# Optimization experiments

Hardware: AMD Instinct MI355X
Metric: run time of the kernel (lower is better)

## Reference

```python
import jax, jax.numpy as jnp
import numpy as np

NSTEP = 5

# Clauses (vals = one-hot satisfying truth value per literal):
#   clause 0: ~S(x) | C(x)          vals: L0=[1,0], L1=[0,1]
#   clause 1: ~F(x,y) | ~S(x) | S(y) vals: L0=[1,0], L1=[1,0], L2=[0,1]
# Message to target literal i (torch influence()):
#   msg = w[r] * einsum over shared vars of prod_j ( q[pn_j] . (1 - vals_j) ) outer t_vals

def setup_inputs() -> dict:
    B, N = 2, 2048
    key = jax.random.key(0)
    k1, k2, k3 = jax.random.split(key, 3)
    return {
        "logits_S": jax.random.normal(k1, (B, N, 2), jnp.float32),
        "logits_C": jax.random.normal(k2, (B, N, 2), jnp.float32),
        "logits_F": jax.random.normal(k3, (B, N, N, 2), jnp.float32),
        "weights": jnp.ones((2,), jnp.float32),
    }


def _messages(qS, qC, qF, weights):
    dt = qS.dtype
    e_true = jnp.array([0.0, 1.0], dtype=dt)   # one-hot: positive literal satisfied
    e_false = jnp.array([1.0, 0.0], dtype=dt)  # one-hot: negated literal satisfied
    w0, w1 = weights[0], weights[1]
    # clause 0: ~S(x) | C(x)
    msg_C = (w0 * qS[..., 1])[..., None] * e_true            # [B,N,2]
    msg_S = (w0 * qC[..., 0])[..., None] * e_false           # [B,N,2]
    # clause 1: ~F(x,y) | ~S(x) | S(y)
    # target F(x,y): (q_S[b,x,true]) * (q_S[b,y,false]) on the 'false' slot of F
    msg_F = (w1 * qS[:, :, None, 1] * qS[:, None, :, 0])[..., None] * e_false  # [B,N,N,2]
    # target ~S(x): sum_y q_F[b,x,y,true] * q_S[b,y,false]
    msg_S = msg_S + (w1 * jnp.einsum('bxy,by->bx', qF[..., 1], qS[..., 0]))[..., None] * e_false
    # target S(y): sum_x q_F[b,x,y,true] * q_S[b,x,true]
    msg_S = msg_S + (w1 * jnp.einsum('bxy,bx->by', qF[..., 1], qS[..., 1]))[..., None] * e_true
    return msg_S, msg_C, msg_F


def reference(logits_S, logits_C, logits_F, weights):
    cur_S, cur_C, cur_F = logits_S, logits_C, logits_F
    for _ in range(NSTEP):
        qS = jax.nn.softmax(cur_S, axis=-1)
        qC = jax.nn.softmax(cur_C, axis=-1)
        qF = jax.nn.softmax(cur_F, axis=-1)
        msg_S, msg_C, msg_F = _messages(qS, qC, qF, weights)
        cur_S = logits_S + msg_S
        cur_C = logits_C + msg_C
        cur_F = logits_F + msg_F
    return (cur_S, cur_C, cur_F)
```

## Files before the change

### kernel.cpp

```cpp
#include <hip/hip_runtime.h>

#define BB 2
#define NN 2048
#define ROWS (BB*NN)
#define RPB 16
#define CSPLIT 4

__device__ __forceinline__ float fsig(float x) {
    float e = __expf(-x);
    return __builtin_amdgcn_rcpf(1.0f + e);
}

__global__ void ksmall(const float* __restrict__ S, const float* __restrict__ C,
                       const float* __restrict__ w,
                       float* __restrict__ r, float* __restrict__ c,
                       const float* __restrict__ aS_prev, float* __restrict__ aS_cur,
                       float* __restrict__ qC0, int first)
{
    int idx = blockIdx.x * blockDim.x + threadIdx.x;
    if (idx >= ROWS) return;
    float w0 = w[0], w1 = w[1];
    float S0 = S[2*idx], S1 = S[2*idx+1];
    float C0 = C[2*idx], C1 = C[2*idx+1];
    float aS, qc;
    if (first) {
        aS = fsig(S1 - S0);
        qc = fsig(C0 - C1);
    } else {
        float ap  = aS_prev[idx];
        float qcp = qC0[idx];
        float s0 = S0 + w0*qcp + w1*r[idx];
        float s1 = S1 + w1*c[idx];
        aS = fsig(s1 - s0);
        qc = fsig(C0 - C1 - w0*ap);
    }
    aS_cur[idx] = aS;
    qC0[idx]    = qc;
    r[idx]      = 0.0f;
    c[idx]      = 0.0f;
}

template<int MODE>
__global__ __launch_bounds__(256) void kbig(
    const float4* __restrict__ F,
    const float* __restrict__ aS_cur, const float* __restrict__ aS_prev,
    const float* __restrict__ w,
    float* __restrict__ r, float* __restrict__ c,
    float4* __restrict__ outF)
{
    const int tid  = threadIdx.x;
    const int j    = blockIdx.x * 256 + tid;
    const int row0 = blockIdx.y * RPB;
    const int b    = row0 >> 11;
    const int lane = tid & 63;
    const float w1 = w[1];

    const float wq0 = 1.0f - aS_cur[b*NN + 2*j];
    const float wq1 = 1.0f - aS_cur[b*NN + 2*j + 1];
    float bp0 = 0.0f, bp1 = 0.0f;
    if (MODE != 0) {
        bp0 = 1.0f - aS_prev[b*NN + 2*j];
        bp1 = 1.0f - aS_prev[b*NN + 2*j + 1];
    }

    float c0 = 0.0f, c1 = 0.0f;

#pragma unroll 2
    for (int i = 0; i < RPB; i++) {
        const int row = row0 + i;
        const int x   = row & (NN - 1);
        const float a_c = aS_cur[b*NN + x];
        float m1 = 0.0f;
        if (MODE != 0) m1 = w1 * aS_prev[b*NN + x];

        const float4 f = F[(size_t)row * (NN/2) + j];
        const float d0 = f.y - f.x;
        const float d1 = f.w - f.z;
        float s0, s1;
        if (MODE == 0) { s0 = fsig(d0); s1 = fsig(d1); }
        else           { s0 = fsig(d0 - m1*bp0); s1 = fsig(d1 - m1*bp1); }

        c0 += s0 * a_c;
        c1 += s1 * a_c;

        if (MODE == 2) {
            const float mw = w1 * a_c;
            float4 o;
            o.x = f.x + mw*wq0;
            o.y = f.y;
            o.z = f.z + mw*wq1;
            o.w = f.w;
            outF[(size_t)row * (NN/2) + j] = o;
        }

        float ra = s0*wq0 + s1*wq1;
#pragma unroll
        for (int off = 32; off > 0; off >>= 1) ra += __shfl_down(ra, off);
        if (lane == 0) atomicAdd(&r[row], ra);
    }

    atomicAdd(&c[b*NN + 2*j],     c0);
    atomicAdd(&c[b*NN + 2*j + 1], c1);
}

__global__ void kfin(const float* __restrict__ S, const float* __restrict__ C,
                     const float* __restrict__ w,
                     const float* __restrict__ r, const float* __restrict__ c,
                     const float* __restrict__ aS4, const float* __restrict__ qC0,
                     float* __restrict__ outS, float* __restrict__ outC)
{
    int idx = blockIdx.x * blockDim.x + threadIdx.x;
    if (idx >= ROWS) return;
    float w0 = w[0], w1 = w[1];
    outS[2*idx]   = S[2*idx]   + w0*qC0[idx] + w1*r[idx];
    outS[2*idx+1] = S[2*idx+1] + w1*c[idx];
    outC[2*idx]   = C[2*idx];
    outC[2*idx+1] = C[2*idx+1] + w0*aS4[idx];
}

extern "C" void kernel_launch(void* const* d_in, const int* in_sizes, int n_in,
                              void* d_out, int out_size, void* d_ws, size_t ws_size,
                              hipStream_t stream)
{
    const float* S = (const float*)d_in[0];
    const float* C = (const float*)d_in[1];
    const float* F = (const float*)d_in[2];
    const float* w = (const float*)d_in[3];
    float* out = (float*)d_out;
    float* ws  = (float*)d_ws;

    float* aSA = ws;
    float* aSB = ws + ROWS;
    float* qC0 = ws + 2*ROWS;
    float* r   = ws + 3*ROWS;
    float* c   = ws + 4*ROWS;

    const float4* F4 = (const float4*)F;
    float* outS = out;
    float* outC = out + 2*ROWS;
    float4* outF = (float4*)(out + 4*ROWS);

    dim3 gs(ROWS/256), bs(256);
    dim3 gb(CSPLIT, ROWS/RPB), bbk(256);

    ksmall<<<gs, bs, 0, stream>>>(S, C, w, r, c, aSB, aSA, qC0, 1);
    kbig<0><<<gb, bbk, 0, stream>>>(F4, aSA, aSB, w, r, c, nullptr);
    ksmall<<<gs, bs, 0, stream>>>(S, C, w, r, c, aSA, aSB, qC0, 0);
    kbig<1><<<gb, bbk, 0, stream>>>(F4, aSB, aSA, w, r, c, nullptr);
    ksmall<<<gs, bs, 0, stream>>>(S, C, w, r, c, aSB, aSA, qC0, 0);
    kbig<1><<<gb, bbk, 0, stream>>>(F4, aSA, aSB, w, r, c, nullptr);
    ksmall<<<gs, bs, 0, stream>>>(S, C, w, r, c, aSA, aSB, qC0, 0);
    kbig<1><<<gb, bbk, 0, stream>>>(F4, aSB, aSA, w, r, c, nullptr);
    ksmall<<<gs, bs, 0, stream>>>(S, C, w, r, c, aSB, aSA, qC0, 0);
    kbig<2><<<gb, bbk, 0, stream>>>(F4, aSA, aSB, w, r, c, outF);
    kfin<<<gs, bs, 0, stream>>>(S, C, w, r, c, aSA, qC0, outS, outC);
}
```

Before: 222.3 us.

## Fuse all iterations into one cooperative kernel caching F differences in LDS

Replaces the eleven launches with a single cooperative kernel of 256 blocks, each owning 16 rows. Each block keeps those rows' F logit differences in shared memory (128KB) so the five iterations read F from HBM once, plus one more read for the final output write. Grid-wide syncs with rotating r/c buffers replace the kernel boundaries, and the S/C updates are recomputed redundantly per block. The cost is grid.sync latency, low occupancy from one large-LDS block per CU, and more redundant small work per block.

```diff
diff --git a/kernel.cpp b/kernel.cpp
--- a/kernel.cpp
+++ b/kernel.cpp
@@ -1,121 +1,142 @@
 #include <hip/hip_runtime.h>
+#include <hip/hip_cooperative_groups.h>
 
-#define BB 2
-#define NN 2048
-#define ROWS (BB*NN)
-#define RPB 16
-#define CSPLIT 4
+namespace cg = cooperative_groups;
+
+#define NN   2048
+#define ROWS 4096
+#define NBLK 256
+#define NTHR 512
+#define RPB  16
+#define SMEM_FLOATS (RPB*NN + 2*NN + NN + 16)
+#define SMEM_BYTES  (SMEM_FLOATS*4)
 
 __device__ __forceinline__ float fsig(float x) {
     float e = __expf(-x);
     return __builtin_amdgcn_rcpf(1.0f + e);
 }
 
-__global__ void ksmall(const float* __restrict__ S, const float* __restrict__ C,
-                       const float* __restrict__ w,
-                       float* __restrict__ r, float* __restrict__ c,
-                       const float* __restrict__ aS_prev, float* __restrict__ aS_cur,
-                       float* __restrict__ qC0, int first)
+__global__ void kfused(const float* __restrict__ S, const float* __restrict__ C,
+                       const float4* __restrict__ F, const float* __restrict__ w,
+                       float* __restrict__ outS, float* __restrict__ outC,
+                       float4* __restrict__ outF,
+                       float* __restrict__ rb, float* __restrict__ cb)
 {
-    int idx = blockIdx.x * blockDim.x + threadIdx.x;
-    if (idx >= ROWS) return;
-    float w0 = w[0], w1 = w[1];
-    float S0 = S[2*idx], S1 = S[2*idx+1];
-    float C0 = C[2*idx], C1 = C[2*idx+1];
-    float aS, qc;
-    if (first) {
-        aS = fsig(S1 - S0);
-        qc = fsig(C0 - C1);
-    } else {
-        float ap  = aS_prev[idx];
-        float qcp = qC0[idx];
-        float s0 = S0 + w0*qcp + w1*r[idx];
-        float s1 = S1 + w1*c[idx];
-        aS = fsig(s1 - s0);
-        qc = fsig(C0 - C1 - w0*ap);
+    cg::grid_group grid = cg::this_grid();
+    extern __shared__ float smem[];
+    float* dF     = smem;
+    float* aSb    = smem + RPB*NN;
+    float* qC0    = aSb + 2*NN;
+    float* rstage = qC0 + NN;
+
+    const int tid  = threadIdx.x;
+    const int blk  = blockIdx.x;
+    const int b    = blk >> 7;
+    const int bloc = blk & 127;
+    const int row0 = blk * RPB;
+    const int base = b * NN;
+    const float w0 = w[0], w1 = w[1];
+    const int lane = tid & 63;
+    const int y0   = 4 * tid;
+
+    if (tid < 48) cb[(tid >> 4) * ROWS + row0 + (tid & 15)] = 0.0f;
+    if (tid < RPB) rstage[tid] = 0.0f;
+    for (int i = tid; i < NN; i += NTHR) {
+        int g = base + i;
+        float2 sv = *(const float2*)&S[2*g];
+        float2 cv = *(const float2*)&C[2*g];
+        aSb[i] = fsig(sv.y - sv.x);
+        qC0[i] = fsig(cv.x - cv.y);
     }
-    aS_cur[idx] = aS;
-    qC0[idx]    = qc;
-    r[idx]      = 0.0f;
-    c[idx]      = 0.0f;
-}
+    for (int u = tid; u < RPB*(NN/2); u += NTHR) {
+        int ir = u >> 10;
+        int j  = u & 1023;
+        float4 f = F[(size_t)(row0 + ir) * (NN/2) + j];
+        *(float2*)&dF[ir*NN + 2*j] = make_float2(f.y - f.x, f.w - f.z);
+    }
+    __threadfence();
+    grid.sync();
 
-template<int MODE>
-__global__ __launch_bounds__(256) void kbig(
-    const float4* __restrict__ F,
-    const float* __restrict__ aS_cur, const float* __restrict__ aS_prev,
-    const float* __restrict__ w,
-    float* __restrict__ r, float* __restrict__ c,
-    float4* __restrict__ outF)
-{
-    const int tid  = threadIdx.x;
-    const int j    = blockIdx.x * 256 + tid;
-    const int row0 = blockIdx.y * RPB;
-    const int b    = row0 >> 11;
-    const int lane = tid & 63;
-    const float w1 = w[1];
+    for (int k = 0; k < 5; k++) {
+        float* aScur  = aSb + (k & 1) * NN;
+        float* aSprev = aSb + ((k & 1) ^ 1) * NN;
+        if (k > 0) {
+            const float* rprev = rb + ((k - 1) & 1) * ROWS;
+            const float* cprev = cb + ((k - 1) % 3) * ROWS;
+            for (int i = tid; i < NN; i += NTHR) {
+                int g = base + i;
+                float2 sv = *(const float2*)&S[2*g];
+                float2 cv = *(const float2*)&C[2*g];
+                float ap = aSprev[i];
+                float s0 = sv.x + w0 * qC0[i] + w1 * rprev[g];
+                float s1 = sv.y + w1 * cprev[g];
+                aScur[i] = fsig(s1 - s0);
+                qC0[i]   = fsig(cv.x - cv.y - w0 * ap);
+            }
+            if (tid < RPB) cb[((k + 1) % 3) * ROWS + row0 + tid] = 0.0f;
+        }
+        __syncthreads();
 
-    const float wq0 = 1.0f - aS_cur[b*NN + 2*j];
-    const float wq1 = 1.0f - aS_cur[b*NN + 2*j + 1];
-    float bp0 = 0.0f, bp1 = 0.0f;
-    if (MODE != 0) {
-        bp0 = 1.0f - aS_prev[b*NN + 2*j];
-        bp1 = 1.0f - aS_prev[b*NN + 2*j + 1];
+        const float wq0 = 1.0f - aScur[y0],     wq1 = 1.0f - aScur[y0 + 1],
+                    wq2 = 1.0f - aScur[y0 + 2], wq3 = 1.0f - aScur[y0 + 3];
+        float bp0 = 0.f, bp1 = 0.f, bp2 = 0.f, bp3 = 0.f;
+        if (k > 0) {
+            bp0 = 1.0f - aSprev[y0];     bp1 = 1.0f - aSprev[y0 + 1];
+            bp2 = 1.0f - aSprev[y0 + 2]; bp3 = 1.0f - aSprev[y0 + 3];
+        }
+        float cacc0 = 0.f, cacc1 = 0.f, cacc2 = 0.f, cacc3 = 0.f;
+#pragma unroll 4
+        for (int ir = 0; ir < RPB; ir++) {
+            const int xl = bloc * RPB + ir;
+            const float a_c = aScur[xl];
+            const float m1  = (k > 0) ? w1 * aSprev[xl] : 0.0f;
+            float4 d = *(float4*)&dF[ir * NN + y0];
+            float s0 = fsig(d.x - m1 * bp0);
+            float s1 = fsig(d.y - m1 * bp1);
+            float s2 = fsig(d.z - m1 * bp2);
+            float s3 = fsig(d.w - m1 * bp3);
+            cacc0 += s0 * a_c; cacc1 += s1 * a_c;
+            cacc2 += s2 * a_c; cacc3 += s3 * a_c;
+            float ra = s0 * wq0 + s1 * wq1 + s2 * wq2 + s3 * wq3;
+#pragma unroll
+            for (int off = 32; off > 0; off >>= 1) ra += __shfl_down(ra, off);
+            if (lane == 0) atomicAdd(&rstage[ir], ra);
+            if (k == 4) {
+                const float mw = w1 * a_c;
+                size_t fo = (size_t)(row0 + ir) * (NN/2) + 2 * tid;
+                float4 fa = F[fo], fb = F[fo + 1];
+                fa.x += mw * wq0; fa.z += mw * wq1;
+                fb.x += mw * wq2; fb.z += mw * wq3;
+                outF[fo] = fa; outF[fo + 1] = fb;
+            }
+        }
+        float* ccur = cb + (k % 3) * ROWS;
+        atomicAdd(&ccur[base + y0],     cacc0);
+        atomicAdd(&ccur[base + y0 + 1], cacc1);
+        atomicAdd(&ccur[base + y0 + 2], cacc2);
+        atomicAdd(&ccur[base + y0 + 3], cacc3);
+        __syncthreads();
+        if (tid < RPB) {
+            rb[(k & 1) * ROWS + row0 + tid] = rstage[tid];
+            rstage[tid] = 0.0f;
+        }
+        __threadfence();
+        grid.sync();
     }
 
-    float c0 = 0.0f, c1 = 0.0f;
-
-#pragma unroll 2
-    for (int i = 0; i < RPB; i++) {
-        const int row = row0 + i;
-        const int x   = row & (NN - 1);
-        const float a_c = aS_cur[b*NN + x];
-        float m1 = 0.0f;
-        if (MODE != 0) m1 = w1 * aS_prev[b*NN + x];
-
-        const float4 f = F[(size_t)row * (NN/2) + j];
-        const float d0 = f.y - f.x;
-        const float d1 = f.w - f.z;
-        float s0, s1;
-        if (MODE == 0) { s0 = fsig(d0); s1 = fsig(d1); }
-        else           { s0 = fsig(d0 - m1*bp0); s1 = fsig(d1 - m1*bp1); }
-
-        c0 += s0 * a_c;
-        c1 += s1 * a_c;
-
-        if (MODE == 2) {
-            const float mw = w1 * a_c;
-            float4 o;
-            o.x = f.x + mw*wq0;
-            o.y = f.y;
-            o.z = f.z + mw*wq1;
-            o.w = f.w;
-            outF[(size_t)row * (NN/2) + j] = o;
-        }
-
-        float ra = s0*wq0 + s1*wq1;
-#pragma unroll
-        for (int off = 32; off > 0; off >>= 1) ra += __shfl_down(ra, off);
-        if (lane == 0) atomicAdd(&r[row], ra);
+    if (tid < RPB) {
+        int g  = row0 + tid;
+        int il = bloc * RPB + tid;
+        float2 sv = *(const float2*)&S[2*g];
+        float2 cv = *(const float2*)&C[2*g];
+        float rv = rb[0 * ROWS + g];
+        float cc = cb[(4 % 3) * ROWS + g];
+        float a4 = aSb[(4 & 1) * NN + il];
+        outS[2*g]     = sv.x + w0 * qC0[il] + w1 * rv;
+        outS[2*g + 1] = sv.y + w1 * cc;
+        outC[2*g]     = cv.x;
+        outC[2*g + 1] = cv.y + w0 * a4;
     }
-
-    atomicAdd(&c[b*NN + 2*j],     c0);
-    atomicAdd(&c[b*NN + 2*j + 1], c1);
-}
-
-__global__ void kfin(const float* __restrict__ S, const float* __restrict__ C,
-                     const float* __restrict__ w,
-                     const float* __restrict__ r, const float* __restrict__ c,
-                     const float* __restrict__ aS4, const float* __restrict__ qC0,
-                     float* __restrict__ outS, float* __restrict__ outC)
-{
-    int idx = blockIdx.x * blockDim.x + threadIdx.x;
-    if (idx >= ROWS) return;
-    float w0 = w[0], w1 = w[1];
-    outS[2*idx]   = S[2*idx]   + w0*qC0[idx] + w1*r[idx];
-    outS[2*idx+1] = S[2*idx+1] + w1*c[idx];
-    outC[2*idx]   = C[2*idx];
-    outC[2*idx+1] = C[2*idx+1] + w0*aS4[idx];
 }
 
 extern "C" void kernel_launch(void* const* d_in, const int* in_sizes, int n_in,
@@ -124,34 +145,28 @@
 {
     const float* S = (const float*)d_in[0];
     const float* C = (const float*)d_in[1];
-    const float* F = (const float*)d_in[2];
+    const float4* F4 = (const float4*)d_in[2];
     const float* w = (const float*)d_in[3];
     float* out = (float*)d_out;
     float* ws  = (float*)d_ws;
 
-    float* aSA = ws;
-    float* aSB = ws + ROWS;
-    float* qC0 = ws + 2*ROWS;
-    float* r   = ws + 3*ROWS;
-    float* c   = ws + 4*ROWS;
+    float* outS = out;
+    float* outC = out + 2 * ROWS;
+    float4* outF = (float4*)(out + 4 * ROWS);
 
-    const float4* F4 = (const float4*)F;
-    float* outS = out;
-    float* outC = out + 2*ROWS;
-    float4* outF = (float4*)(out + 4*ROWS);
+    float* rb = ws;
+    float* cb = ws + 2 * ROWS;
 
-    dim3 gs(ROWS/256), bs(256);
-    dim3 gb(CSPLIT, ROWS/RPB), bbk(256);
+    static bool attr_set = false;
+    if (!attr_set) {
+        hipFuncSetAttribute((const void*)kfused,
+                            hipFuncAttributeMaxDynamicSharedMemorySize, SMEM_BYTES);
+        attr_set = true;
+    }
 
-    ksmall<<<gs, bs, 0, stream>>>(S, C, w, r, c, aSB, aSA, qC0, 1);
-    kbig<0><<<gb, bbk, 0, stream>>>(F4, aSA, aSB, w, r, c, nullptr);
-    ksmall<<<gs, bs, 0, stream>>>(S, C, w, r, c, aSA, aSB, qC0, 0);
-    kbig<1><<<gb, bbk, 0, stream>>>(F4, aSB, aSA, w, r, c, nullptr);
-    ksmall<<<gs, bs, 0, stream>>>(S, C, w, r, c, aSB, aSA, qC0, 0);
-    kbig<1><<<gb, bbk, 0, stream>>>(F4, aSA, aSB, w, r, c, nullptr);
-    ksmall<<<gs, bs, 0, stream>>>(S, C, w, r, c, aSA, aSB, qC0, 0);
-    kbig<1><<<gb, bbk, 0, stream>>>(F4, aSB, aSA, w, r, c, nullptr);
-    ksmall<<<gs, bs, 0, stream>>>(S, C, w, r, c, aSB, aSA, qC0, 0);
-    kbig<2><<<gb, bbk, 0, stream>>>(F4, aSA, aSB, w, r, c, outF);
-    kfin<<<gs, bs, 0, stream>>>(S, C, w, r, c, aSA, qC0, outS, outC);
+    void* args[] = { (void*)&S, (void*)&C, (void*)&F4, (void*)&w,
+                     (void*)&outS, (void*)&outC, (void*)&outF,
+                     (void*)&rb, (void*)&cb };
+    hipLaunchCooperativeKernel((const void*)kfused, dim3(NBLK), dim3(NTHR),
+                               args, SMEM_BYTES, stream);
 }
```

After: 637.8 us. +186.9%, slower.
